# Kernel tuning notes

Measured on AMD Instinct MI355X. Metric: run time of the kernel, lower is better.

The kernel has to match this reference:

```python
import jax, jax.numpy as jnp
import numpy as np
import math

B, N = 1, 512
C_S, C_Z, C_H, H = 384, 128, 16, 12
P_Q, P_V, NBINS = 4, 8, 64
OUT_DIM = H * (C_H + P_V * 4 + C_Z)


def setup_inputs() -> dict:
    key = jax.random.key(0)
    ks = jax.random.split(key, 16)
    def rn(k, shape, scale=1.0):
        return jax.random.normal(k, shape, dtype=jnp.float32) * scale
    rotations, _ = jnp.linalg.qr(rn(ks[3], (B, N, 3, 3)))  # orthogonal frames
    w = 0.02
    return {
        "s": rn(ks[0], (B, N, C_S)),
        "z": rn(ks[1], (B, N, N, C_Z)),
        "translations": rn(ks[2], (B, N, 3), 10.0),  # spread over ~0-32 A bins
        "rotations": rotations,
        "Wq": rn(ks[4], (C_S, H * C_H), w), "bq": jnp.zeros((H * C_H,), jnp.float32),
        "Wk": rn(ks[5], (C_S, H * C_H), w), "bk": jnp.zeros((H * C_H,), jnp.float32),
        "Wv": rn(ks[6], (C_S, H * C_H), w), "bv": jnp.zeros((H * C_H,), jnp.float32),
        "Wqp": rn(ks[7], (C_S, H * P_Q * 3), w), "bqp": jnp.zeros((H * P_Q * 3,), jnp.float32),
        "Wkp": rn(ks[8], (C_S, H * P_Q * 3), w), "bkp": jnp.zeros((H * P_Q * 3,), jnp.float32),
        "Wvp": rn(ks[9], (C_S, H * P_V * 3), w), "bvp": jnp.zeros((H * P_V * 3,), jnp.float32),
        "Wb": rn(ks[10], (C_Z, H), w), "bb": jnp.zeros((H,), jnp.float32),
        "emb": rn(ks[11], (NBINS, H), w),
        "scale_logits": jnp.zeros((3, H), jnp.float32),
        "head_weights": jnp.ones((H,), jnp.float32),
        "Wout": rn(ks[12], (OUT_DIM, C_S), w), "bout": jnp.zeros((C_S,), jnp.float32),
    }


def reference(s, z, translations, rotations, Wq, bq, Wk, bk, Wv, bv, Wqp, bqp, Wkp, bkp, Wvp, bvp, Wb, bb, emb, scale_logits, head_weights, Wout, bout):
    b, n, _ = s.shape
    t = translations
    q = (s @ Wq + bq).reshape(b, n, H, C_H)
    k = (s @ Wk + bk).reshape(b, n, H, C_H)
    v = (s @ Wv + bv).reshape(b, n, H, C_H)
    q_pts = (s @ Wqp + bqp).reshape(b, n, H, P_Q, 3)
    k_pts = (s @ Wkp + bkp).reshape(b, n, H, P_Q, 3)
    v_pts = (s @ Wvp + bvp).reshape(b, n, H, P_V, 3)
    # local -> global frame
    q_g = jnp.einsum('bnij,bnhpj->bnhpi', rotations, q_pts) + t[:, :, None, None, :]
    k_g = jnp.einsum('bnij,bnhpj->bnhpi', rotations, k_pts) + t[:, :, None, None, :]
    v_g = jnp.einsum('bnij,bnhpj->bnhpi', rotations, v_pts) + t[:, :, None, None, :]
    scalar_logits = jnp.einsum('bnhc,bmhc->bnmh', q, k) / math.sqrt(C_H)  # [b,n,m,h]
    point_dist = jnp.sum((q_g[:, :, None] - k_g[:, None]) ** 2, axis=-1)  # [b,n,m,h,p]
    point_logits = -0.5 * jnp.sum(point_dist, axis=-1) * head_weights[None, None, None, :]
    pair_bias = z @ Wb + bb  # [b,n,m,h]
    pair_dist = jnp.linalg.norm(t[:, :, None, :] - t[:, None, :, :], axis=-1)  # [b,n,m]
    edges = jnp.linspace(0.0, 32.0, NBINS + 1)
    bins = jnp.clip(jnp.searchsorted(edges, pair_dist, side='left') - 1, 0, NBINS - 1)
    dist_bias = emb[bins]  # [b,n,m,h]
    scales = jnp.stack([
        (pair_dist <= 5.0).astype(s.dtype),
        ((pair_dist > 5.0) & (pair_dist <= 15.0)).astype(s.dtype),
        jnp.ones_like(pair_dist),
    ], axis=-1)  # [b,n,m,3]
    per_head = jax.nn.softmax(scale_logits, axis=0)  # [3,h]
    multiscale = jnp.einsum('bnms,sh->bnmh', scales, per_head)
    logits = scalar_logits + point_logits + pair_bias + dist_bias + multiscale
    attn = jax.nn.softmax(logits.astype(jnp.float32), axis=2).astype(s.dtype)  # over m
    out_scalar = jnp.einsum('bnmh,bmhc->bnhc', attn, v)
    out_pts_g = jnp.einsum('bnmh,bmhpi->bnhpi', attn, v_g)
    # global -> local frame (R^T applied)
    out_pts_l = jnp.einsum('bnji,bnhpj->bnhpi', rotations, out_pts_g - t[:, :, None, None, :])
    out_norms = jnp.linalg.norm(out_pts_l, axis=-1)  # [b,n,h,p]
    pair_feat = jnp.einsum('bnmh,bnmc->bnhc', attn, z)
    feats = jnp.concatenate([
        out_scalar,
        out_pts_l.reshape(b, n, H, P_V * 3),
        out_norms,
        pair_feat,
    ], axis=-1).reshape(b, n, -1)  # [b,n,OUT_DIM]
    return feats @ Wout + bout
```

## Files before the change

### kernel.cpp

```cpp
#include <hip/hip_runtime.h>

#define NTOK 512
#define CS 384
#define CZ 128
#define CH 16
#define HN 12
#define PQ 4
#define PV 8
#define FEAT_DIM 2112
#define HSEG 176

__global__ __launch_bounds__(256) void k_proj(
    const float* __restrict__ s,
    const float* __restrict__ Wq,  const float* __restrict__ bq,
    const float* __restrict__ Wk,  const float* __restrict__ bk,
    const float* __restrict__ Wv,  const float* __restrict__ bv,
    const float* __restrict__ Wqp, const float* __restrict__ bqp,
    const float* __restrict__ Wkp, const float* __restrict__ bkp,
    const float* __restrict__ Wvp, const float* __restrict__ bvp,
    float* __restrict__ qs, float* __restrict__ ksT, float* __restrict__ vs,
    float* __restrict__ raw_g)
{
    __shared__ float s_l[16 * CS];
    const int t  = threadIdx.x;
    const int n0 = blockIdx.x * 16;

    const float4* sg  = (const float4*)(s + (size_t)n0 * CS);
    float4*       sl4 = (float4*)s_l;
#pragma unroll
    for (int j = 0; j < 6; ++j) sl4[j * 256 + t] = sg[j * 256 + t];
    __syncthreads();

    const int col = blockIdx.y * 64 + (t & 63);
    const int tq  = t >> 6;

    const float *W, *bv_;
    int lc, nc;
    if (col < 192)      { W = Wq;  bv_ = bq;  lc = col;       nc = 192; }
    else if (col < 384) { W = Wk;  bv_ = bk;  lc = col - 192; nc = 192; }
    else if (col < 576) { W = Wv;  bv_ = bv;  lc = col - 384; nc = 192; }
    else if (col < 720) { W = Wqp; bv_ = bqp; lc = col - 576; nc = 144; }
    else if (col < 864) { W = Wkp; bv_ = bkp; lc = col - 720; nc = 144; }
    else                { W = Wvp; bv_ = bvp; lc = col - 864; nc = 288; }

    const float* Wp   = W + lc;
    const float* srow = s_l + tq * 4 * CS;
    float a0, a1, a2, a3;
    a0 = a1 = a2 = a3 = bv_[lc];
#pragma unroll 8
    for (int k = 0; k < CS; ++k) {
        float w = Wp[(size_t)k * nc];
        a0 += srow[k] * w;
        a1 += srow[CS + k] * w;
        a2 += srow[2 * CS + k] * w;
        a3 += srow[3 * CS + k] * w;
    }

    const int n = n0 + tq * 4;
    if (col < 192) {
        qs[(size_t)(n + 0) * 192 + lc] = a0;
        qs[(size_t)(n + 1) * 192 + lc] = a1;
        qs[(size_t)(n + 2) * 192 + lc] = a2;
        qs[(size_t)(n + 3) * 192 + lc] = a3;
    } else if (col < 384) {
        float* p = ksT + (size_t)lc * NTOK + n;
        p[0] = a0; p[1] = a1; p[2] = a2; p[3] = a3;
    } else if (col < 576) {
        vs[(size_t)(n + 0) * 192 + lc] = a0;
        vs[(size_t)(n + 1) * 192 + lc] = a1;
        vs[(size_t)(n + 2) * 192 + lc] = a2;
        vs[(size_t)(n + 3) * 192 + lc] = a3;
    } else {
        const int pc = col - 576;
        raw_g[(size_t)(n + 0) * 576 + pc] = a0;
        raw_g[(size_t)(n + 1) * 576 + pc] = a1;
        raw_g[(size_t)(n + 2) * 576 + pc] = a2;
        raw_g[(size_t)(n + 3) * 576 + pc] = a3;
    }
}

__global__ __launch_bounds__(256) void k_frame(
    const float* __restrict__ raw_g,
    const float* __restrict__ trans,
    const float* __restrict__ rot,
    float* __restrict__ qg, float* __restrict__ kgT, float* __restrict__ vg,
    float* __restrict__ transT)
{
    const int e = blockIdx.x * 256 + threadIdx.x;
    if (e < 512 * 576) {
        const int n = e / 576, loc = e % 576;
        const int i = loc % 3, base = loc - i;
        const float* rp = raw_g + (size_t)n * 576 + base;
        float x0 = rp[0], x1 = rp[1], x2 = rp[2];
        const float* R = rot + (size_t)n * 9 + i * 3;
        float v = trans[(size_t)n * 3 + i] + R[0] * x0 + R[1] * x1 + R[2] * x2;
        if (loc < 144)      qg[(size_t)n * 144 + loc] = v;
        else if (loc < 288) kgT[(size_t)(loc - 144) * NTOK + n] = v;
        else                vg[(size_t)n * 288 + loc - 288] = v;
    } else {
        const int idx = e - 512 * 576;
        if (idx < 3 * NTOK) {
            const int m = idx / 3, i = idx % 3;
            transT[(size_t)i * NTOK + m] = trans[(size_t)m * 3 + i];
        }
    }
}

__global__ __launch_bounds__(256) void k_bias(
    const float* __restrict__ z,
    const float* __restrict__ Wb,
    const float* __restrict__ bbv,
    float* __restrict__ bias)
{
    __shared__ float a_l[64 * 132];
    __shared__ float wb_l[CZ * HN];
    __shared__ float bb_l[HN];
    const int t = threadIdx.x;
    for (int i = t; i < CZ * HN; i += 256) wb_l[i] = Wb[i];
    if (t < HN) bb_l[t] = bbv[t];

    const float4* zg = (const float4*)(z + (size_t)blockIdx.x * 64 * CZ);
#pragma unroll
    for (int j = 0; j < 8; ++j) {
        const int f4i = j * 256 + t;
        const int row = f4i >> 5, c4 = f4i & 31;
        *(float4*)&a_l[row * 132 + c4 * 4] = zg[f4i];
    }
    __syncthreads();

    const int row = t & 63;
    const int hg  = t >> 6;
    float acc0 = 0.f, acc1 = 0.f, acc2 = 0.f;
    const float4* ar = (const float4*)&a_l[row * 132];
    const float*  wr = wb_l + hg * 3;
#pragma unroll 8
    for (int k4 = 0; k4 < 32; ++k4) {
        float4 zv = ar[k4];
        float zs[4] = {zv.x, zv.y, zv.z, zv.w};
#pragma unroll
        for (int e = 0; e < 4; ++e) {
            const float* w = wr + (k4 * 4 + e) * HN;
            acc0 += zs[e] * w[0];
            acc1 += zs[e] * w[1];
            acc2 += zs[e] * w[2];
        }
    }
    const int grow = blockIdx.x * 64 + row;
    const int n = grow >> 9, m = grow & 511;
    const int h = hg * 3;
    bias[((size_t)n * HN + h + 0) * NTOK + m] = acc0 + bb_l[h + 0];
    bias[((size_t)n * HN + h + 1) * NTOK + m] = acc1 + bb_l[h + 1];
    bias[((size_t)n * HN + h + 2) * NTOK + m] = acc2 + bb_l[h + 2];
}

__global__ __launch_bounds__(256) void k_attn(
    const float* __restrict__ qs, const float* __restrict__ ksT,
    const float* __restrict__ qg, const float* __restrict__ kgT,
    const float* __restrict__ trans, const float* __restrict__ transT,
    const float* __restrict__ emb,
    const float* __restrict__ slog,
    const float* __restrict__ hw,
    float* __restrict__ attn)
{
    const int n = blockIdx.x, h = blockIdx.y, t = threadIdx.x;
    __shared__ float ql[CH];
    __shared__ float qgl[12];
    __shared__ float tl[3];
    __shared__ float ph[3];
    __shared__ float red[8];
    __shared__ float emb_l[64];
    if (t < CH)       ql[t] = qs[(size_t)n * 192 + h * CH + t];
    else if (t < 28)  qgl[t - 16] = qg[(size_t)n * 144 + h * 12 + (t - 16)];
    else if (t < 31)  tl[t - 28] = trans[(size_t)n * 3 + (t - 28)];
    else if (t == 31) {
        float s0 = slog[0 * HN + h], s1 = slog[1 * HN + h], s2 = slog[2 * HN + h];
        float mx = fmaxf(s0, fmaxf(s1, s2));
        float e0 = expf(s0 - mx), e1 = expf(s1 - mx), e2 = expf(s2 - mx);
        float inv = 1.f / (e0 + e1 + e2);
        ph[0] = e0 * inv; ph[1] = e1 * inv; ph[2] = e2 * inv;
    } else if (t >= 64 && t < 128) {
        emb_l[t - 64] = emb[(size_t)(t - 64) * HN + h];
    }
    __syncthreads();

    const float hwv = hw[h];
    float* arow = attn + ((size_t)n * HN + h) * NTOK;
    const float* ksh = ksT + (size_t)h * CH * NTOK;
    const float* kgh = kgT + (size_t)h * 12 * NTOK;
    float lg[2];
#pragma unroll
    for (int r = 0; r < 2; ++r) {
        const int m = t + r * 256;
        float sc = 0.f;
#pragma unroll
        for (int c = 0; c < CH; ++c)
            sc += ql[c] * ksh[(size_t)c * NTOK + m];
        sc *= 0.25f;
        float sd = 0.f;
#pragma unroll
        for (int i = 0; i < 12; ++i) {
            float d = qgl[i] - kgh[(size_t)i * NTOK + m];
            sd += d * d;
        }
        float pl = -0.5f * sd * hwv;
        float dx = tl[0] - transT[m];
        float dy = tl[1] - transT[NTOK + m];
        float dz = tl[2] - transT[2 * NTOK + m];
        float dist = sqrtf(dx * dx + dy * dy + dz * dz);
        int bin = (int)ceilf(dist * 2.f) - 1;
        bin = min(63, max(0, bin));
        float db = emb_l[bin];
        float ms = ph[2] + (dist <= 5.f ? ph[0] : 0.f) + ((dist > 5.f && dist <= 15.f) ? ph[1] : 0.f);
        lg[r] = sc + pl + arow[m] + db + ms;
    }

    float mx = fmaxf(lg[0], lg[1]);
    for (int off = 32; off; off >>= 1) mx = fmaxf(mx, __shfl_down(mx, off));
    if ((t & 63) == 0) red[t >> 6] = mx;
    __syncthreads();
    if (t == 0) red[4] = fmaxf(fmaxf(red[0], red[1]), fmaxf(red[2], red[3]));
    __syncthreads();
    mx = red[4];
    float e0 = expf(lg[0] - mx), e1 = expf(lg[1] - mx);
    float sm = e0 + e1;
    for (int off = 32; off; off >>= 1) sm += __shfl_down(sm, off);
    if ((t & 63) == 0) red[t >> 6] = sm;
    __syncthreads();
    if (t == 0) red[5] = red[0] + red[1] + red[2] + red[3];
    __syncthreads();
    const float inv = 1.f / red[5];
    arow[t] = e0 * inv;
    arow[t + 256] = e1 * inv;
}

__global__ __launch_bounds__(256) void k_outmm(
    const float* __restrict__ attn,
    const float* __restrict__ vs, const float* __restrict__ vg,
    const float* __restrict__ trans,
    const float* __restrict__ rot,
    float* __restrict__ feats)
{
    __shared__ float As_t[64][65];
    __shared__ float Vs[64][40];
    __shared__ float out_l[64 * 40];
    __shared__ float Rl[64][9];
    __shared__ float tl[64][3];
    const int t   = threadIdx.x;
    const int gn0 = blockIdx.x * 64;
    const int h   = blockIdx.y;

    const int slab  = t >> 6;
    const int w     = t & 63;
    const int n0l   = (w >> 2) * 4;
    const int j0    = (w & 3) * 10;

    float acc[4][10];
#pragma unroll
    for (int i = 0; i < 4; ++i)
#pragma unroll
        for (int k = 0; k < 10; ++k) acc[i][k] = 0.f;

    for (int step = 0; step < 8; ++step) {
        const int mb = step * 64;
        __syncthreads();
#pragma unroll
        for (int jj = 0; jj < 4; ++jj) {
            const int f = t + jj * 256;
            const int n_loc = f >> 4, c4 = f & 15;
            float4 a = *(const float4*)&attn[(((size_t)(gn0 + n_loc)) * HN + h) * NTOK + mb + c4 * 4];
            As_t[c4 * 4 + 0][n_loc] = a.x;
            As_t[c4 * 4 + 1][n_loc] = a.y;
            As_t[c4 * 4 + 2][n_loc] = a.z;
            As_t[c4 * 4 + 3][n_loc] = a.w;
        }
#pragma unroll
        for (int jj = 0; jj < 10; ++jj) {
            const int f = t + jj * 256;
            const int m_loc = f / 40, jv = f % 40;
            float v;
            if (jv < 16) v = vs[(size_t)(mb + m_loc) * 192 + h * 16 + jv];
            else         v = vg[(size_t)(mb + m_loc) * 288 + h * 24 + (jv - 16)];
            Vs[m_loc][jv] = v;
        }
        __syncthreads();
#pragma unroll
        for (int mi = 0; mi < 16; ++mi) {
            const int m = slab * 16 + mi;
            float4 a  = *(const float4*)&As_t[m][n0l];
            float2 v0 = *(const float2*)&Vs[m][j0 + 0];
            float2 v1 = *(const float2*)&Vs[m][j0 + 2];
            float2 v2 = *(const float2*)&Vs[m][j0 + 4];
            float2 v3 = *(const float2*)&Vs[m][j0 + 6];
            float2 v4 = *(const float2*)&Vs[m][j0 + 8];
            const float av[4]  = {a.x, a.y, a.z, a.w};
            const float vv[10] = {v0.x, v0.y, v1.x, v1.y, v2.x,
                                  v2.y, v3.x, v3.y, v4.x, v4.y};
#pragma unroll
            for (int i = 0; i < 4; ++i)
#pragma unroll
                for (int k = 0; k < 10; ++k)
                    acc[i][k] += av[i] * vv[k];
        }
    }

    for (int s = 0; s < 4; ++s) {
        __syncthreads();
        if (slab == s) {
#pragma unroll
            for (int i = 0; i < 4; ++i)
#pragma unroll
                for (int k = 0; k < 10; ++k) {
                    float* p = &out_l[(n0l + i) * 40 + j0 + k];
                    if (s == 0) *p = acc[i][k];
                    else        *p += acc[i][k];
                }
        }
    }
    for (int i = t; i < 64 * 12; i += 256) {
        const int n_loc = i / 12, r = i % 12;
        if (r < 9) Rl[n_loc][r] = rot[(size_t)(gn0 + n_loc) * 9 + r];
        else       tl[n_loc][r - 9] = trans[(size_t)(gn0 + n_loc) * 3 + (r - 9)];
    }
    __syncthreads();

    for (int f = t; f < 64 * 48; f += 256) {
        const int n_loc = f / 48, j = f % 48;
        const float* sh = &out_l[n_loc * 40];
        float* fp = feats + (size_t)(gn0 + n_loc) * FEAT_DIM + h * HSEG;
        const float* R = Rl[n_loc];
        const float* tv = tl[n_loc];
        if (j < 16) {
            fp[j] = sh[j];
        } else if (j < 40) {
            const int jj = j - 16, p = jj / 3, i = jj % 3;
            float val = 0.f;
#pragma unroll
            for (int q = 0; q < 3; ++q) val += R[q * 3 + i] * (sh[16 + p * 3 + q] - tv[q]);
            fp[16 + jj] = val;
        } else {
            const int p = j - 40;
            float s2 = 0.f;
#pragma unroll
            for (int i = 0; i < 3; ++i) {
                float val = 0.f;
#pragma unroll
                for (int q = 0; q < 3; ++q) val += R[q * 3 + i] * (sh[16 + p * 3 + q] - tv[q]);
                s2 += val * val;
            }
            fp[40 + p] = sqrtf(s2);
        }
    }
}

__global__ __launch_bounds__(256) void k_pairfeat(
    const float* __restrict__ attn,
    const float* __restrict__ z,
    float* __restrict__ feats)
{
    __shared__ float a_l[HN * NTOK];
    const int n = blockIdx.x, t = threadIdx.x;
    for (int i = t; i < HN * NTOK; i += 256) a_l[i] = attn[(size_t)n * HN * NTOK + i];
    __syncthreads();

    const int c2 = (t & 63) * 2;
    const int hb = (t >> 6) * 3;
    float acc[3][2] = {{0.f, 0.f}, {0.f, 0.f}, {0.f, 0.f}};
    const float* zp = z + (size_t)n * NTOK * CZ + c2;
    const float* ap = a_l + hb * NTOK;
#pragma unroll 8
    for (int m = 0; m < NTOK; ++m) {
        float2 zv = *(const float2*)(zp + (size_t)m * CZ);
#pragma unroll
        for (int u = 0; u < 3; ++u) {
            float a = ap[u * NTOK + m];
            acc[u][0] += a * zv.x;
            acc[u][1] += a * zv.y;
        }
    }
#pragma unroll
    for (int u = 0; u < 3; ++u) {
        float2 r = make_float2(acc[u][0], acc[u][1]);
        *(float2*)&feats[(size_t)n * FEAT_DIM + (hb + u) * HSEG + 48 + c2] = r;
    }
}

#define KT 16
__global__ __launch_bounds__(256) void k_outproj(
    const float* __restrict__ feats,
    const float* __restrict__ Wout,
    const float* __restrict__ bout,
    float* __restrict__ out)
{
    __shared__ float As[KT][64];
    __shared__ float Bs[KT][64];
    const int t  = threadIdx.x;
    const int n0 = blockIdx.x * 64;
    const int j0 = blockIdx.y * 64;
    const int k0 = blockIdx.z * HSEG;

    const int arow = t >> 2, akq = (t & 3) * 4;
    const int bkk  = t >> 4, bjq = (t & 15) * 4;
    const int tr   = t >> 4, tc  = t & 15;

    float acc[4][4] = {{0.f}};
    for (int s = 0; s < 11; ++s) {
        const int ks = k0 + s * KT;
        float4 a4 = *(const float4*)&feats[(size_t)(n0 + arow) * FEAT_DIM + ks + akq];
        float4 b4 = *(const float4*)&Wout[(size_t)(ks + bkk) * 384 + j0 + bjq];
        __syncthreads();
        As[akq + 0][arow] = a4.x;
        As[akq + 1][arow] = a4.y;
        As[akq + 2][arow] = a4.z;
        As[akq + 3][arow] = a4.w;
        *(float4*)&Bs[bkk][bjq] = b4;
        __syncthreads();
#pragma unroll
        for (int kk = 0; kk < KT; ++kk) {
            float4 av = *(const float4*)&As[kk][tr * 4];
            float4 bv = *(const float4*)&Bs[kk][tc * 4];
            acc[0][0] += av.x * bv.x; acc[0][1] += av.x * bv.y;
            acc[0][2] += av.x * bv.z; acc[0][3] += av.x * bv.w;
            acc[1][0] += av.y * bv.x; acc[1][1] += av.y * bv.y;
            acc[1][2] += av.y * bv.z; acc[1][3] += av.y * bv.w;
            acc[2][0] += av.z * bv.x; acc[2][1] += av.z * bv.y;
            acc[2][2] += av.z * bv.z; acc[2][3] += av.z * bv.w;
            acc[3][0] += av.w * bv.x; acc[3][1] += av.w * bv.y;
            acc[3][2] += av.w * bv.z; acc[3][3] += av.w * bv.w;
        }
    }

    const bool addb = (blockIdx.z == 0);
#pragma unroll
    for (int i = 0; i < 4; ++i) {
        const int row = n0 + tr * 4 + i;
#pragma unroll
        for (int jj = 0; jj < 4; ++jj) {
            const int col = j0 + tc * 4 + jj;
            float v = acc[i][jj];
            if (addb) v += bout[col];
            atomicAdd(&out[(size_t)row * 384 + col], v);
        }
    }
}

extern "C" void kernel_launch(void* const* d_in, const int* in_sizes, int n_in,
                              void* d_out, int out_size, void* d_ws, size_t ws_size,
                              hipStream_t stream) {
    const float* s     = (const float*)d_in[0];
    const float* z     = (const float*)d_in[1];
    const float* trans = (const float*)d_in[2];
    const float* rot   = (const float*)d_in[3];
    const float* Wq    = (const float*)d_in[4];
    const float* bq    = (const float*)d_in[5];
    const float* Wk    = (const float*)d_in[6];
    const float* bk    = (const float*)d_in[7];
    const float* Wv    = (const float*)d_in[8];
    const float* bv    = (const float*)d_in[9];
    const float* Wqp   = (const float*)d_in[10];
    const float* bqp   = (const float*)d_in[11];
    const float* Wkp   = (const float*)d_in[12];
    const float* bkp   = (const float*)d_in[13];
    const float* Wvp   = (const float*)d_in[14];
    const float* bvp   = (const float*)d_in[15];
    const float* Wb    = (const float*)d_in[16];
    const float* bb    = (const float*)d_in[17];
    const float* emb   = (const float*)d_in[18];
    const float* slog  = (const float*)d_in[19];
    const float* hw    = (const float*)d_in[20];
    const float* Wout  = (const float*)d_in[21];
    const float* bout  = (const float*)d_in[22];

    float* W = (float*)d_ws;
    float* qs     = W;
    float* ksT    = qs + 98304;
    float* vs     = ksT + 98304;
    float* qg     = vs + 98304;
    float* kgT    = qg + 73728;
    float* vg     = kgT + 73728;
    float* transT = vg + 147456;
    float* bias   = transT + 1536;
    float* feats  = bias + 3145728;
    float* raw_g  = feats + 1081344;

    k_proj<<<dim3(32, 18), 256, 0, stream>>>(s, Wq, bq, Wk, bk, Wv, bv,
                                             Wqp, bqp, Wkp, bkp, Wvp, bvp,
                                             qs, ksT, vs, raw_g);
    k_frame<<<1158, 256, 0, stream>>>(raw_g, trans, rot, qg, kgT, vg, transT);
    k_bias<<<4096, 256, 0, stream>>>(z, Wb, bb, bias);
    k_attn<<<dim3(512, 12), 256, 0, stream>>>(qs, ksT, qg, kgT, trans, transT,
                                              emb, slog, hw, bias);
    k_outmm<<<dim3(8, 12), 256, 0, stream>>>(bias, vs, vg, trans, rot, feats);
    k_pairfeat<<<512, 256, 0, stream>>>(bias, z, feats);
    hipMemsetAsync(d_out, 0, (size_t)NTOK * 384 * sizeof(float), stream);
    k_outproj<<<dim3(8, 6, 12), 256, 0, stream>>>(feats, Wout, bout, (float*)d_out);
}
```

Before: 415.9 us.

## Retile projection, bias, outmm and pairfeat kernels for better reuse and occupancy

The projection kernel now stages weight tiles in shared memory with coalesced float4 loads instead of strided per-thread global reads. The bias kernel pads its shared rows to 133 to avoid bank conflicts. The outmm kernel halves its row tile to double the block count. The pairfeat kernel splits the m dimension across warps, so each thread reads z once for all 12 heads instead of each warp re-reading z for 3 heads, then reduces the partial sums in shared memory. These changes target uncoalesced weight loads, repeated z traffic and low block counts, at the cost of extra barriers and more registers.

```diff
diff --git a/kernel.cpp b/kernel.cpp
--- a/kernel.cpp
+++ b/kernel.cpp
@@ -22,6 +22,7 @@
     float* __restrict__ raw_g)
 {
     __shared__ float s_l[16 * CS];
+    __shared__ float Ws[16][64];
     const int t  = threadIdx.x;
     const int n0 = blockIdx.x * 16;
 
@@ -29,31 +30,46 @@
     float4*       sl4 = (float4*)s_l;
 #pragma unroll
     for (int j = 0; j < 6; ++j) sl4[j * 256 + t] = sg[j * 256 + t];
-    __syncthreads();
 
     const int col = blockIdx.y * 64 + (t & 63);
     const int tq  = t >> 6;
-
-    const float *W, *bv_;
-    int lc, nc;
-    if (col < 192)      { W = Wq;  bv_ = bq;  lc = col;       nc = 192; }
-    else if (col < 384) { W = Wk;  bv_ = bk;  lc = col - 192; nc = 192; }
-    else if (col < 576) { W = Wv;  bv_ = bv;  lc = col - 384; nc = 192; }
-    else if (col < 720) { W = Wqp; bv_ = bqp; lc = col - 576; nc = 144; }
-    else if (col < 864) { W = Wkp; bv_ = bkp; lc = col - 720; nc = 144; }
-    else                { W = Wvp; bv_ = bvp; lc = col - 864; nc = 288; }
-
-    const float* Wp   = W + lc;
-    const float* srow = s_l + tq * 4 * CS;
+    const float* bv_;
+    int lc;
+    if (col < 192)      { bv_ = bq;  lc = col;       }
+    else if (col < 384) { bv_ = bk;  lc = col - 192; }
+    else if (col < 576) { bv_ = bv;  lc = col - 384; }
+    else if (col < 720) { bv_ = bqp; lc = col - 576; }
+    else if (col < 864) { bv_ = bkp; lc = col - 720; }
+    else                { bv_ = bvp; lc = col - 864; }
+
+    const int kk_s = t >> 4, cq = t & 15;
+    const int gcol = blockIdx.y * 64 + cq * 4;
+    const float* Wsrc; int lcs, ncs;
+    if (gcol < 192)      { Wsrc = Wq;  lcs = gcol;       ncs = 192; }
+    else if (gcol < 384) { Wsrc = Wk;  lcs = gcol - 192; ncs = 192; }
+    else if (gcol < 576) { Wsrc = Wv;  lcs = gcol - 384; ncs = 192; }
+    else if (gcol < 720) { Wsrc = Wqp; lcs = gcol - 576; ncs = 144; }
+    else if (gcol < 864) { Wsrc = Wkp; lcs = gcol - 720; ncs = 144; }
+    else                 { Wsrc = Wvp; lcs = gcol - 864; ncs = 288; }
+
     float a0, a1, a2, a3;
     a0 = a1 = a2 = a3 = bv_[lc];
-#pragma unroll 8
-    for (int k = 0; k < CS; ++k) {
-        float w = Wp[(size_t)k * nc];
-        a0 += srow[k] * w;
-        a1 += srow[CS + k] * w;
-        a2 += srow[2 * CS + k] * w;
-        a3 += srow[3 * CS + k] * w;
+    __syncthreads();
+
+    for (int ks = 0; ks < CS; ks += 16) {
+        float4 w4 = *(const float4*)&Wsrc[(size_t)(ks + kk_s) * ncs + lcs];
+        __syncthreads();
+        *(float4*)&Ws[kk_s][cq * 4] = w4;
+        __syncthreads();
+        const float* srow = s_l + tq * 4 * CS + ks;
+#pragma unroll
+        for (int kk = 0; kk < 16; ++kk) {
+            float w = Ws[kk][t & 63];
+            a0 += srow[kk] * w;
+            a1 += srow[CS + kk] * w;
+            a2 += srow[2 * CS + kk] * w;
+            a3 += srow[3 * CS + kk] * w;
+        }
     }
 
     const int n = n0 + tq * 4;
@@ -112,7 +128,7 @@
     const float* __restrict__ bbv,
     float* __restrict__ bias)
 {
-    __shared__ float a_l[64 * 132];
+    __shared__ float a_l[64 * 133];
     __shared__ float wb_l[CZ * HN];
     __shared__ float bb_l[HN];
     const int t = threadIdx.x;
@@ -124,26 +140,24 @@
     for (int j = 0; j < 8; ++j) {
         const int f4i = j * 256 + t;
         const int row = f4i >> 5, c4 = f4i & 31;
-        *(float4*)&a_l[row * 132 + c4 * 4] = zg[f4i];
+        float4 v = zg[f4i];
+        float* dst = &a_l[row * 133 + c4 * 4];
+        dst[0] = v.x; dst[1] = v.y; dst[2] = v.z; dst[3] = v.w;
     }
     __syncthreads();
 
     const int row = t & 63;
     const int hg  = t >> 6;
     float acc0 = 0.f, acc1 = 0.f, acc2 = 0.f;
-    const float4* ar = (const float4*)&a_l[row * 132];
-    const float*  wr = wb_l + hg * 3;
+    const float* ar = &a_l[row * 133];
+    const float* wr = wb_l + hg * 3;
 #pragma unroll 8
-    for (int k4 = 0; k4 < 32; ++k4) {
-        float4 zv = ar[k4];
-        float zs[4] = {zv.x, zv.y, zv.z, zv.w};
-#pragma unroll
-        for (int e = 0; e < 4; ++e) {
-            const float* w = wr + (k4 * 4 + e) * HN;
-            acc0 += zs[e] * w[0];
-            acc1 += zs[e] * w[1];
-            acc2 += zs[e] * w[2];
-        }
+    for (int c = 0; c < CZ; ++c) {
+        float zc = ar[c];
+        const float* w = wr + c * HN;
+        acc0 += zc * w[0];
+        acc1 += zc * w[1];
+        acc2 += zc * w[2];
     }
     const int grow = blockIdx.x * 64 + row;
     const int n = grow >> 9, m = grow & 511;
@@ -240,31 +254,31 @@
     const float* __restrict__ rot,
     float* __restrict__ feats)
 {
-    __shared__ float As_t[64][65];
+    __shared__ float As_t[64][33];
     __shared__ float Vs[64][40];
-    __shared__ float out_l[64 * 40];
-    __shared__ float Rl[64][9];
-    __shared__ float tl[64][3];
+    __shared__ float out_l[32 * 40];
+    __shared__ float Rl[32][9];
+    __shared__ float tl[32][3];
     const int t   = threadIdx.x;
-    const int gn0 = blockIdx.x * 64;
+    const int gn0 = blockIdx.x * 32;
     const int h   = blockIdx.y;
 
     const int slab  = t >> 6;
     const int w     = t & 63;
-    const int n0l   = (w >> 2) * 4;
-    const int j0    = (w & 3) * 10;
-
-    float acc[4][10];
+    const int n0l   = (w >> 3) * 4;
+    const int j0    = (w & 7) * 5;
+
+    float acc[4][5];
 #pragma unroll
     for (int i = 0; i < 4; ++i)
 #pragma unroll
-        for (int k = 0; k < 10; ++k) acc[i][k] = 0.f;
+        for (int k = 0; k < 5; ++k) acc[i][k] = 0.f;
 
     for (int step = 0; step < 8; ++step) {
         const int mb = step * 64;
         __syncthreads();
 #pragma unroll
-        for (int jj = 0; jj < 4; ++jj) {
+        for (int jj = 0; jj < 2; ++jj) {
             const int f = t + jj * 256;
             const int n_loc = f >> 4, c4 = f & 15;
             float4 a = *(const float4*)&attn[(((size_t)(gn0 + n_loc)) * HN + h) * NTOK + mb + c4 * 4];
@@ -286,19 +300,15 @@
 #pragma unroll
         for (int mi = 0; mi < 16; ++mi) {
             const int m = slab * 16 + mi;
-            float4 a  = *(const float4*)&As_t[m][n0l];
-            float2 v0 = *(const float2*)&Vs[m][j0 + 0];
-            float2 v1 = *(const float2*)&Vs[m][j0 + 2];
-            float2 v2 = *(const float2*)&Vs[m][j0 + 4];
-            float2 v3 = *(const float2*)&Vs[m][j0 + 6];
-            float2 v4 = *(const float2*)&Vs[m][j0 + 8];
-            const float av[4]  = {a.x, a.y, a.z, a.w};
-            const float vv[10] = {v0.x, v0.y, v1.x, v1.y, v2.x,
-                                  v2.y, v3.x, v3.y, v4.x, v4.y};
+            float4 a = *(const float4*)&As_t[m][n0l];
+            float vv[5];
+#pragma unroll
+            for (int k = 0; k < 5; ++k) vv[k] = Vs[m][j0 + k];
+            const float av[4] = {a.x, a.y, a.z, a.w};
 #pragma unroll
             for (int i = 0; i < 4; ++i)
 #pragma unroll
-                for (int k = 0; k < 10; ++k)
+                for (int k = 0; k < 5; ++k)
                     acc[i][k] += av[i] * vv[k];
         }
     }
@@ -309,21 +319,21 @@
 #pragma unroll
             for (int i = 0; i < 4; ++i)
 #pragma unroll
-                for (int k = 0; k < 10; ++k) {
+                for (int k = 0; k < 5; ++k) {
                     float* p = &out_l[(n0l + i) * 40 + j0 + k];
                     if (s == 0) *p = acc[i][k];
                     else        *p += acc[i][k];
                 }
         }
     }
-    for (int i = t; i < 64 * 12; i += 256) {
+    for (int i = t; i < 32 * 12; i += 256) {
         const int n_loc = i / 12, r = i % 12;
         if (r < 9) Rl[n_loc][r] = rot[(size_t)(gn0 + n_loc) * 9 + r];
         else       tl[n_loc][r - 9] = trans[(size_t)(gn0 + n_loc) * 3 + (r - 9)];
     }
     __syncthreads();
 
-    for (int f = t; f < 64 * 48; f += 256) {
+    for (int f = t; f < 32 * 48; f += 256) {
         const int n_loc = f / 48, j = f % 48;
         const float* sh = &out_l[n_loc * 40];
         float* fp = feats + (size_t)(gn0 + n_loc) * FEAT_DIM + h * HSEG;
@@ -358,29 +368,44 @@
     float* __restrict__ feats)
 {
     __shared__ float a_l[HN * NTOK];
+    __shared__ float out_l[HN * CZ];
     const int n = blockIdx.x, t = threadIdx.x;
     for (int i = t; i < HN * NTOK; i += 256) a_l[i] = attn[(size_t)n * HN * NTOK + i];
     __syncthreads();
 
-    const int c2 = (t & 63) * 2;
-    const int hb = (t >> 6) * 3;
-    float acc[3][2] = {{0.f, 0.f}, {0.f, 0.f}, {0.f, 0.f}};
-    const float* zp = z + (size_t)n * NTOK * CZ + c2;
-    const float* ap = a_l + hb * NTOK;
-#pragma unroll 8
-    for (int m = 0; m < NTOK; ++m) {
+    const int slab = t >> 6, lane = t & 63;
+    const int c2 = lane * 2;
+    float acc[HN][2];
+#pragma unroll
+    for (int h = 0; h < HN; ++h) { acc[h][0] = 0.f; acc[h][1] = 0.f; }
+
+    const float* zp = z + (size_t)n * NTOK * CZ + (size_t)slab * 128 * CZ + c2;
+    const float* ap = a_l + slab * 128;
+#pragma unroll 4
+    for (int m = 0; m < 128; ++m) {
         float2 zv = *(const float2*)(zp + (size_t)m * CZ);
 #pragma unroll
-        for (int u = 0; u < 3; ++u) {
-            float a = ap[u * NTOK + m];
-            acc[u][0] += a * zv.x;
-            acc[u][1] += a * zv.y;
-        }
-    }
-#pragma unroll
-    for (int u = 0; u < 3; ++u) {
-        float2 r = make_float2(acc[u][0], acc[u][1]);
-        *(float2*)&feats[(size_t)n * FEAT_DIM + (hb + u) * HSEG + 48 + c2] = r;
+        for (int h = 0; h < HN; ++h) {
+            float a = ap[h * NTOK + m];
+            acc[h][0] += a * zv.x;
+            acc[h][1] += a * zv.y;
+        }
+    }
+    for (int s = 0; s < 4; ++s) {
+        __syncthreads();
+        if (slab == s) {
+#pragma unroll
+            for (int h = 0; h < HN; ++h) {
+                float* p = &out_l[h * CZ + c2];
+                if (s == 0) { p[0] = acc[h][0]; p[1] = acc[h][1]; }
+                else        { p[0] += acc[h][0]; p[1] += acc[h][1]; }
+            }
+        }
+    }
+    __syncthreads();
+    for (int i = t; i < HN * CZ; i += 256) {
+        const int h = i >> 7, c = i & 127;
+        feats[(size_t)n * FEAT_DIM + h * HSEG + 48 + c] = out_l[i];
     }
 }
 
@@ -489,7 +514,7 @@
     k_bias<<<4096, 256, 0, stream>>>(z, Wb, bb, bias);
     k_attn<<<dim3(512, 12), 256, 0, stream>>>(qs, ksT, qg, kgT, trans, transT,
                                               emb, slog, hw, bias);
-    k_outmm<<<dim3(8, 12), 256, 0, stream>>>(bias, vs, vg, trans, rot, feats);
+    k_outmm<<<dim3(16, 12), 256, 0, stream>>>(bias, vs, vg, trans, rot, feats);
     k_pairfeat<<<512, 256, 0, stream>>>(bias, z, feats);
     hipMemsetAsync(d_out, 0, (size_t)NTOK * 384 * sizeof(float), stream);
     k_outproj<<<dim3(8, 6, 12), 256, 0, stream>>>(feats, Wout, bout, (float*)d_out);
```

Result: faster. 400.2 us (-3.8%).
